# Performance work log

Hardware: AMD Instinct MI355X
Metric: run time of the kernel (lower is better)

## Reference

```python
import jax, jax.numpy as jnp
import numpy as np

# --- hash-grid / Field hyperparams (from init_kwargs defaults) ---
L = 16            # n_levels
F = 2             # n_features_per_level
LOG2_T = 19
T = 1 << LOG2_T   # hashmap size per level
NMIN = 16         # base_resolution
MAXRES = 512
SCALE = 1.0
HIDDEN = 32
OUT_DIM = 1
N = 2_000_000
B = float(np.exp(np.log(MAXRES * SCALE / NMIN) / (L - 1)))  # per_level_scale
PRIMES = jnp.array([1, 2654435761, 805459861], dtype=jnp.uint32)
# 8 corner offsets of the unit cube, (8,3)
CORNERS = jnp.array([[(c >> 0) & 1, (c >> 1) & 1, (c >> 2) & 1] for c in range(8)], dtype=jnp.uint32)


def hash_encode(xn, table):
    """xn: (N,3) in [0,1]; table: (L,T,F). Returns (N, L*F)."""
    feats = []
    for l in range(L):  # fixed small loop over levels
        s = NMIN * (B ** l) - 1.0          # tcnn-style grid scale
        pos = xn * s                        # (N,3)
        p0 = jnp.floor(pos)
        w = pos - p0                        # trilinear fracs, (N,3)
        p0i = p0.astype(jnp.uint32)
        corner = p0i[:, None, :] + CORNERS[None, :, :]          # (N,8,3)
        h = corner * PRIMES                                      # (N,8,3) uint32 wrap-mul
        idx = (h[..., 0] ^ h[..., 1] ^ h[..., 2]) & jnp.uint32(T - 1)  # (N,8)
        # trilinear weights per corner: prod over dims of w or (1-w)
        cw = jnp.where(CORNERS[None, :, :] == 1, w[:, None, :], 1.0 - w[:, None, :])
        cw = cw.prod(axis=-1)                                    # (N,8)
        g = table[l][idx.astype(jnp.int32)]                      # (N,8,F)
        feats.append(jnp.einsum('ncf,nc->nf', g, cw))            # (N,F)
    return jnp.concatenate(feats, axis=-1)                       # (N, L*F)


def setup_inputs() -> dict:
    key = jax.random.key(0)
    ks = jax.random.split(key, 8)
    x = jax.random.uniform(ks[0], (N, 3), jnp.float32)  # coords in [0,1) subset of [-scale,scale]
    table = jax.random.normal(ks[1], (L, T, F), jnp.float32) * 1e-2
    W0 = jax.random.normal(ks[2], (L * F + 3, HIDDEN), jnp.float32) * 0.1
    b0 = jnp.zeros((HIDDEN,), jnp.float32)
    W1 = jax.random.normal(ks[3], (HIDDEN, HIDDEN), jnp.float32) * 0.1
    b1 = jnp.zeros((HIDDEN,), jnp.float32)
    Wout = jax.random.normal(ks[4], (HIDDEN, OUT_DIM), jnp.float32) * 0.1
    bout = jnp.zeros((OUT_DIM,), jnp.float32)
    return {"x": x, "table": table, "W0": W0, "b0": b0, "W1": W1, "b1": b1, "Wout": Wout, "bout": bout}


def reference(x, table, W0, b0, W1, b1, Wout, bout):
    # density(): normalize coords to [0,1]
    xn = (x + SCALE) / (2.0 * SCALE)
    # back_prop=0: encoder sees detached coords
    h = hash_encode(jax.lax.stop_gradient(xn), table)   # (N, L*F)
    feat = jnp.concatenate([xn, h], axis=-1)            # (N, 35)  torch.cat([x, h], 1)
    h1 = jax.nn.elu(feat @ W0 + b0)
    h2 = jax.nn.elu(h1 @ W1 + b1)
    out = h2 @ Wout + bout                              # (N, 1)
    return out
```

## Files before the change

kernel.cpp:

```cpp
#include <hip/hip_runtime.h>
#include <hip/hip_fp16.h>
#include <cmath>

#define LVL   16
#define NDENSE 11
#define NHASH  (LVL - NDENSE)
#define TSIZE (1u << 19)
#define TMASK (TSIZE - 1u)
#define HID   32
#define PRIME1 2654435761u
#define PRIME2 805459861u
#define FSTRIDE 72

struct Scales { float s[LVL]; };
struct DenseInfo {
    int X0[NDENSE];
    int dim[NDENSE];
    int dimsq[NDENSE];
    int base[NDENSE];
    int eoff[NDENSE + 1];
};

typedef _Float16 f16x8 __attribute__((ext_vector_type(8)));
typedef float    f32x4 __attribute__((ext_vector_type(4)));
typedef float    f32x2 __attribute__((ext_vector_type(2)));
typedef unsigned u32x4 __attribute__((ext_vector_type(4)));

__device__ __forceinline__ float elu_f(float v) {
    return v > 0.0f ? v : expm1f(v);
}
__device__ __forceinline__ unsigned sel4(u32x4 v, unsigned s) {
    unsigned lo = (s & 1) ? v.y : v.x;
    unsigned hi = (s & 1) ? v.w : v.z;
    return (s & 2) ? hi : lo;
}
__device__ __forceinline__ unsigned hashed(unsigned cx, unsigned cy, unsigned cz) {
    return (cx ^ (cy * PRIME1) ^ (cz * PRIME2)) & TMASK;
}

__device__ __forceinline__ unsigned enc8(float v) {
    unsigned short t = __half_as_ushort(__float2half_rn(v * 0.0625f));
    unsigned m = (unsigned)(t & 0x7FFF) + 0x40u;
    return ((t >> 8) & 0x80u) | (m >> 7);
}
__device__ __forceinline__ float2 dec2(unsigned hw) {
    unsigned h2 = ((hw & 0x8000u) << 16) | ((hw & 0x7F00u) << 15)
                | ((hw & 0x80u)   << 8)  | ((hw & 0x7Fu)   << 7);
    __half2 hh; __builtin_memcpy(&hh, &h2, 4);
    return __half22float2(hh);
}

__global__ __launch_bounds__(256)
void convert_hash8(const f32x2* __restrict__ src, unsigned short* __restrict__ dst)
{
    int i = blockIdx.x * blockDim.x + threadIdx.x;
    if (i >= NHASH * (int)TSIZE) return;
    int l = NDENSE + i / (int)TSIZE;
    int s = i & (int)TMASK;
    f32x2 v = src[(size_t)l * TSIZE + s];
    dst[i] = (unsigned short)(enc8(v.x) | (enc8(v.y) << 8));
}

__global__ __launch_bounds__(256)
void dense_prep8(const float* __restrict__ table, u32x4* __restrict__ dtab,
                 DenseInfo di)
{
    int e = blockIdx.x * blockDim.x + threadIdx.x;
    if (e >= di.eoff[NDENSE]) return;
    int l = 0;
#pragma unroll
    for (int k = 1; k < NDENSE; ++k) if (e >= di.eoff[k]) l = k;
    int le = e - di.eoff[l];
    int D = di.dim[l];
    int ex = le % D; int r = le / D;
    int ey = r % D;  int ez = r / D;
    unsigned cx = (unsigned)(di.X0[l] + ex);
    unsigned cy = (unsigned)(di.X0[l] + ey);
    unsigned cz = (unsigned)(di.X0[l] + ez);
    const f32x2* __restrict__ tl = (const f32x2*)table + (size_t)l * TSIZE;
    f32x2 c0 = tl[hashed(cx,      cy,      cz)];
    f32x2 c1 = tl[hashed(cx + 1u, cy,      cz)];
    f32x2 c2 = tl[hashed(cx,      cy + 1u, cz)];
    f32x2 c3 = tl[hashed(cx + 1u, cy + 1u, cz)];
    f32x2 c4 = tl[hashed(cx,      cy,      cz + 1u)];
    f32x2 c5 = tl[hashed(cx + 1u, cy,      cz + 1u)];
    f32x2 c6 = tl[hashed(cx,      cy + 1u, cz + 1u)];
    f32x2 c7 = tl[hashed(cx + 1u, cy + 1u, cz + 1u)];
    u32x4 q;
    q.x = enc8(c0.x) | (enc8(c0.y) << 8) | (enc8(c1.x) << 16) | (enc8(c1.y) << 24);
    q.y = enc8(c2.x) | (enc8(c2.y) << 8) | (enc8(c3.x) << 16) | (enc8(c3.y) << 24);
    q.z = enc8(c4.x) | (enc8(c4.y) << 8) | (enc8(c5.x) << 16) | (enc8(c5.y) << 24);
    q.w = enc8(c6.x) | (enc8(c6.y) << 8) | (enc8(c7.x) << 16) | (enc8(c7.y) << 24);
    dtab[di.base[l] + le] = q;
}

__global__ void prep_frags(const float* __restrict__ W0, const float* __restrict__ W1,
                           const float* __restrict__ Wout, _Float16* __restrict__ frags)
{
    int idx = blockIdx.x * blockDim.x + threadIdx.x;
    if (idx >= 14*64*8) return;
    int f = idx >> 9;
    int rem = idx & 511;
    int lane = rem >> 3;
    int j = rem & 7;
    int q = lane >> 4;
    int nn = lane & 15;

    float w = 0.0f;
    bool lo;
    if (f < 8) {
        int part = f >> 2, kt = (f >> 1) & 1, nt = f & 1;
        int k = kt*32 + q*8 + j;
        int ncol = nt*16 + nn;
        float val = 0.0f;
        if (k < 32)      val = W0[(3 + k)  * HID + ncol];
        else if (k < 35) val = W0[(k - 32) * HID + ncol];
        else if (k < 38) val = W0[(k - 35) * HID + ncol];
        w = val; lo = (part == 1);
    } else if (f < 12) {
        int part = (f - 8) >> 1, nt = (f - 8) & 1;
        int k = q*8 + j;
        int ncol = nt*16 + nn;
        w = W1[k * HID + ncol]; lo = (part == 1);
    } else {
        int part = f - 12;
        int k = q*8 + j;
        w = (nn == 0) ? Wout[k] : 0.0f; lo = (part == 1);
    }
    _Float16 hi = (_Float16)w;
    frags[idx] = lo ? (_Float16)(w - (float)hi) : hi;
}

__global__ __launch_bounds__(256, 4)
void fused_mfma_kernel(const float* __restrict__ x, const u32x4* __restrict__ htab8,
                       const u32x4* __restrict__ dtab,
                       const float* __restrict__ b0, const float* __restrict__ b1,
                       const float* __restrict__ bout, const _Float16* __restrict__ fragbuf,
                       float* __restrict__ out, int n, Scales sc, DenseInfo di)
{
    __shared__ __attribute__((aligned(16))) _Float16 featL[256 * FSTRIDE];
    __shared__ __attribute__((aligned(16))) _Float16 h1h[4][16*32], h1l[4][16*32];
    __shared__ __attribute__((aligned(16))) _Float16 h2h[4][16*32], h2l[4][16*32];

    const int t = threadIdx.x;
    const int pbase = blockIdx.x * 256;
    const int p  = pbase + t;
    const int pc = p < n ? p : n - 1;

    const float xn0 = (x[3*pc+0] + 1.0f) * 0.5f;
    const float xn1 = (x[3*pc+1] + 1.0f) * 0.5f;
    const float xn2 = (x[3*pc+2] + 1.0f) * 0.5f;

    _Float16* row = &featL[t * FSTRIDE];
    {
        _Float16 h0 = (_Float16)xn0, h1_ = (_Float16)xn1, h2_ = (_Float16)xn2;
        row[32] = h0; row[33] = h1_; row[34] = h2_;
        row[35] = (_Float16)(xn0 - (float)h0);
        row[36] = (_Float16)(xn1 - (float)h1_);
        row[37] = (_Float16)(xn2 - (float)h2_);
#pragma unroll
        for (int k = 38; k < 64; ++k) row[k] = (_Float16)0.0f;
    }

#pragma unroll
    for (int l = 0; l < NDENSE; ++l) {
        const float s = sc.s[l];
        float px = xn0 * s, py = xn1 * s, pz = xn2 * s;
        float fx = floorf(px), fy = floorf(py), fz = floorf(pz);
        float wx = px - fx, wy = py - fy, wz = pz - fz;
        int D = di.dim[l], Dsq = di.dimsq[l], X0 = di.X0[l];
        int cx = (int)fx - X0, cy = (int)fy - X0, cz = (int)fz - X0;
        cx = min(max(cx, 0), D - 1);
        cy = min(max(cy, 0), D - 1);
        cz = min(max(cz, 0), D - 1);
        u32x4 Q = dtab[(size_t)(di.base[l] + cx + cy * D + cz * Dsq)];
        float2 a00 = dec2(Q.x & 0xFFFFu), a10 = dec2(Q.x >> 16);
        float2 a01 = dec2(Q.y & 0xFFFFu), a11 = dec2(Q.y >> 16);
        float2 c00 = dec2(Q.z & 0xFFFFu), c10 = dec2(Q.z >> 16);
        float2 c01 = dec2(Q.w & 0xFFFFu), c11 = dec2(Q.w >> 16);
        float ux = 1.0f - wx, uy = 1.0f - wy, uz = 1.0f - wz;
        float b0x = uy*(ux*a00.x + wx*a10.x) + wy*(ux*a01.x + wx*a11.x);
        float b0y = uy*(ux*a00.y + wx*a10.y) + wy*(ux*a01.y + wx*a11.y);
        float b1x = uy*(ux*c00.x + wx*c10.x) + wy*(ux*c01.x + wx*c11.x);
        float b1y = uy*(ux*c00.y + wx*c10.y) + wy*(ux*c01.y + wx*c11.y);
        row[2*l + 0] = (_Float16)(16.0f * (uz * b0x + wz * b1x));
        row[2*l + 1] = (_Float16)(16.0f * (uz * b0y + wz * b1y));
    }

#pragma unroll
    for (int l = NDENSE; l < LVL; ++l) {
        const u32x4* __restrict__ qt = htab8 + ((size_t)(l - NDENSE) * TSIZE >> 3);
        const float s = sc.s[l];
        float px = xn0 * s, py = xn1 * s, pz = xn2 * s;
        float fx = floorf(px), fy = floorf(py), fz = floorf(pz);
        float wx = px - fx, wy = py - fy, wz = pz - fz;
        unsigned x0 = (unsigned)fx, y0 = (unsigned)fy, z0 = (unsigned)fz;
        unsigned hy0 = y0 * PRIME1, hy1 = hy0 + PRIME1;
        unsigned hz0 = z0 * PRIME2, hz1 = hz0 + PRIME2;
        unsigned b00 = hy0 ^ hz0, b10 = hy1 ^ hz0, b01 = hy0 ^ hz1, b11 = hy1 ^ hz1;
        unsigned i0 = (x0 ^ b00) & TMASK;
        unsigned i1 = (x0 ^ b10) & TMASK;
        unsigned i2 = (x0 ^ b01) & TMASK;
        unsigned i3 = (x0 ^ b11) & TMASK;

        u32x4 Q0 = qt[i0 >> 3];
        u32x4 Q1 = qt[i1 >> 3];
        u32x4 Q2 = qt[i2 >> 3];
        u32x4 Q3 = qt[i3 >> 3];

        unsigned dm = (x0 ^ (x0 + 1u)) & TMASK;
        unsigned j0 = i0 ^ dm, j1 = i1 ^ dm, j2 = i2 ^ dm, j3 = i3 ^ dm;

        unsigned hc0, hc1, hc2, hc3;
        if ((x0 & 7u) == 7u) {
            u32x4 R0 = qt[j0 >> 3];
            u32x4 R1 = qt[j1 >> 3];
            u32x4 R2 = qt[j2 >> 3];
            u32x4 R3 = qt[j3 >> 3];
            unsigned d0 = sel4(R0, (j0 >> 1) & 3), d1 = sel4(R1, (j1 >> 1) & 3);
            unsigned d2 = sel4(R2, (j2 >> 1) & 3), d3 = sel4(R3, (j3 >> 1) & 3);
            hc0 = (j0 & 1) ? (d0 >> 16) : (d0 & 0xFFFFu);
            hc1 = (j1 & 1) ? (d1 >> 16) : (d1 & 0xFFFFu);
            hc2 = (j2 & 1) ? (d2 >> 16) : (d2 & 0xFFFFu);
            hc3 = (j3 & 1) ? (d3 >> 16) : (d3 & 0xFFFFu);
        } else {
            unsigned d0 = sel4(Q0, (j0 >> 1) & 3), d1 = sel4(Q1, (j1 >> 1) & 3);
            unsigned d2 = sel4(Q2, (j2 >> 1) & 3), d3 = sel4(Q3, (j3 >> 1) & 3);
            hc0 = (j0 & 1) ? (d0 >> 16) : (d0 & 0xFFFFu);
            hc1 = (j1 & 1) ? (d1 >> 16) : (d1 & 0xFFFFu);
            hc2 = (j2 & 1) ? (d2 >> 16) : (d2 & 0xFFFFu);
            hc3 = (j3 & 1) ? (d3 >> 16) : (d3 & 0xFFFFu);
        }
        unsigned e0 = sel4(Q0, (i0 >> 1) & 3), e1 = sel4(Q1, (i1 >> 1) & 3);
        unsigned e2 = sel4(Q2, (i2 >> 1) & 3), e3 = sel4(Q3, (i3 >> 1) & 3);
        unsigned ha0 = (i0 & 1) ? (e0 >> 16) : (e0 & 0xFFFFu);
        unsigned ha1 = (i1 & 1) ? (e1 >> 16) : (e1 & 0xFFFFu);
        unsigned ha2 = (i2 & 1) ? (e2 >> 16) : (e2 & 0xFFFFu);
        unsigned ha3 = (i3 & 1) ? (e3 >> 16) : (e3 & 0xFFFFu);

        float2 A0 = dec2(ha0), A1 = dec2(ha1), A2 = dec2(ha2), A3 = dec2(ha3);
        float2 C0 = dec2(hc0), C1 = dec2(hc1), C2 = dec2(hc2), C3 = dec2(hc3);
        float ux = 1.0f - wx, uy = 1.0f - wy, uz = 1.0f - wz;
        float w00 = uy*uz, w10 = wy*uz, w01 = uy*wz, w11 = wy*wz;
        float f0 = ux * (w00*A0.x + w10*A1.x + w01*A2.x + w11*A3.x)
                 + wx * (w00*C0.x + w10*C1.x + w01*C2.x + w11*C3.x);
        float f1 = ux * (w00*A0.y + w10*A1.y + w01*A2.y + w11*A3.y)
                 + wx * (w00*C0.y + w10*C1.y + w01*C2.y + w11*C3.y);

        row[2*l + 0] = (_Float16)(16.0f * f0);
        row[2*l + 1] = (_Float16)(16.0f * f1);
    }
    __syncthreads();

    const int l = t & 63, w = t >> 6;
    const int q = l >> 4, nn = l & 15;

    const f16x8* FB = (const f16x8*)fragbuf;
    f16x8 B0h00 = FB[0*64 + l], B0h01 = FB[1*64 + l];
    f16x8 B0h10 = FB[2*64 + l], B0h11 = FB[3*64 + l];
    f16x8 B0l00 = FB[4*64 + l], B0l01 = FB[5*64 + l];
    f16x8 B0l10 = FB[6*64 + l], B0l11 = FB[7*64 + l];
    f16x8 B1h0  = FB[8*64 + l], B1h1  = FB[9*64 + l];
    f16x8 B1l0  = FB[10*64 + l], B1l1 = FB[11*64 + l];
    f16x8 B2h   = FB[12*64 + l], B2l  = FB[13*64 + l];

    float bias00 = b0[nn], bias01 = b0[16 + nn];
    float bias10 = b1[nn], bias11 = b1[16 + nn];
    float biasO  = (nn == 0) ? bout[0] : 0.0f;

    _Float16* H1h = &h1h[w][0]; _Float16* H1l = &h1l[w][0];
    _Float16* H2h = &h2h[w][0]; _Float16* H2l = &h2l[w][0];

#pragma unroll
    for (int mt = 0; mt < 4; ++mt) {
        const int mrow = w*64 + mt*16 + nn;
        const _Float16* arow = &featL[mrow * FSTRIDE];

        f16x8 A0 = *(const f16x8*)(arow + q*8);
        f16x8 A1 = *(const f16x8*)(arow + 32 + q*8);
        f32x4 c0 = {bias00, bias00, bias00, bias00};
        f32x4 c1 = {bias01, bias01, bias01, bias01};
        c0 = __builtin_amdgcn_mfma_f32_16x16x32_f16(A0, B0h00, c0, 0, 0, 0);
        c0 = __builtin_amdgcn_mfma_f32_16x16x32_f16(A1, B0h10, c0, 0, 0, 0);
        c0 = __builtin_amdgcn_mfma_f32_16x16x32_f16(A0, B0l00, c0, 0, 0, 0);
        c0 = __builtin_amdgcn_mfma_f32_16x16x32_f16(A1, B0l10, c0, 0, 0, 0);
        c1 = __builtin_amdgcn_mfma_f32_16x16x32_f16(A0, B0h01, c1, 0, 0, 0);
        c1 = __builtin_amdgcn_mfma_f32_16x16x32_f16(A1, B0h11, c1, 0, 0, 0);
        c1 = __builtin_amdgcn_mfma_f32_16x16x32_f16(A0, B0l01, c1, 0, 0, 0);
        c1 = __builtin_amdgcn_mfma_f32_16x16x32_f16(A1, B0l11, c1, 0, 0, 0);

#pragma unroll
        for (int r = 0; r < 4; ++r) {
            int m = q*4 + r;
            float e0 = elu_f(c0[r]);
            _Float16 hh = (_Float16)e0;
            H1h[m*32 + nn]      = hh;
            H1l[m*32 + nn]      = (_Float16)(e0 - (float)hh);
            float e1 = elu_f(c1[r]);
            hh = (_Float16)e1;
            H1h[m*32 + 16 + nn] = hh;
            H1l[m*32 + 16 + nn] = (_Float16)(e1 - (float)hh);
        }

        f16x8 Ah = *(const f16x8*)(H1h + nn*32 + q*8);
        f16x8 Al = *(const f16x8*)(H1l + nn*32 + q*8);
        f32x4 d0 = {bias10, bias10, bias10, bias10};
        f32x4 d1 = {bias11, bias11, bias11, bias11};
        d0 = __builtin_amdgcn_mfma_f32_16x16x32_f16(Ah, B1h0, d0, 0, 0, 0);
        d0 = __builtin_amdgcn_mfma_f32_16x16x32_f16(Ah, B1l0, d0, 0, 0, 0);
        d0 = __builtin_amdgcn_mfma_f32_16x16x32_f16(Al, B1h0, d0, 0, 0, 0);
        d1 = __builtin_amdgcn_mfma_f32_16x16x32_f16(Ah, B1h1, d1, 0, 0, 0);
        d1 = __builtin_amdgcn_mfma_f32_16x16x32_f16(Ah, B1l1, d1, 0, 0, 0);
        d1 = __builtin_amdgcn_mfma_f32_16x16x32_f16(Al, B1h1, d1, 0, 0, 0);

#pragma unroll
        for (int r = 0; r < 4; ++r) {
            int m = q*4 + r;
            float e0 = elu_f(d0[r]);
            _Float16 hh = (_Float16)e0;
            H2h[m*32 + nn]      = hh;
            H2l[m*32 + nn]      = (_Float16)(e0 - (float)hh);
            float e1 = elu_f(d1[r]);
            hh = (_Float16)e1;
            H2h[m*32 + 16 + nn] = hh;
            H2l[m*32 + 16 + nn] = (_Float16)(e1 - (float)hh);
        }

        f16x8 A2h = *(const f16x8*)(H2h + nn*32 + q*8);
        f16x8 A2l = *(const f16x8*)(H2l + nn*32 + q*8);
        f32x4 c3 = {biasO, biasO, biasO, biasO};
        c3 = __builtin_amdgcn_mfma_f32_16x16x32_f16(A2h, B2h, c3, 0, 0, 0);
        c3 = __builtin_amdgcn_mfma_f32_16x16x32_f16(A2h, B2l, c3, 0, 0, 0);
        c3 = __builtin_amdgcn_mfma_f32_16x16x32_f16(A2l, B2h, c3, 0, 0, 0);

        if (nn == 0) {
            int pout = pbase + w*64 + mt*16 + q*4;
#pragma unroll
            for (int r = 0; r < 4; ++r)
                if (pout + r < n) out[pout + r] = c3[r];
        }
    }
}

__device__ __forceinline__ float2 enc_level_f32(float xn0, float xn1, float xn2, float s,
                                                const float2* __restrict__ tb)
{
    float px = xn0 * s, py = xn1 * s, pz = xn2 * s;
    float fx = floorf(px), fy = floorf(py), fz = floorf(pz);
    float wx = px - fx, wy = py - fy, wz = pz - fz;
    unsigned x0 = (unsigned)fx, y0 = (unsigned)fy, z0 = (unsigned)fz;
    unsigned hy0 = y0 * PRIME1, hy1 = hy0 + PRIME1;
    unsigned hz0 = z0 * PRIME2, hz1 = hz0 + PRIME2;
    unsigned b00 = hy0 ^ hz0, b10 = hy1 ^ hz0, b01 = hy0 ^ hz1, b11 = hy1 ^ hz1;
    float2 g000 = tb[( x0       ^ b00) & TMASK];
    float2 g100 = tb[((x0 + 1u) ^ b00) & TMASK];
    float2 g010 = tb[( x0       ^ b10) & TMASK];
    float2 g110 = tb[((x0 + 1u) ^ b10) & TMASK];
    float2 g001 = tb[( x0       ^ b01) & TMASK];
    float2 g101 = tb[((x0 + 1u) ^ b01) & TMASK];
    float2 g011 = tb[( x0       ^ b11) & TMASK];
    float2 g111 = tb[((x0 + 1u) ^ b11) & TMASK];
    float ux = 1.0f - wx, uy = 1.0f - wy, uz = 1.0f - wz;
    float c00 = uy*uz, c10 = wy*uz, c01 = uy*wz, c11 = wy*wz;
    float f0 = ux * (c00*g000.x + c10*g010.x + c01*g001.x + c11*g011.x)
             + wx * (c00*g100.x + c10*g110.x + c01*g101.x + c11*g111.x);
    float f1 = ux * (c00*g000.y + c10*g010.y + c01*g001.y + c11*g011.y)
             + wx * (c00*g100.y + c10*g110.y + c01*g101.y + c11*g111.y);
    return make_float2(f0, f1);
}

__global__ __launch_bounds__(256, 4)
void fused_fp32_kernel(const float* __restrict__ x, const float* __restrict__ table,
                       const float* __restrict__ W0, const float* __restrict__ b0,
                       const float* __restrict__ W1, const float* __restrict__ b1,
                       const float* __restrict__ Wout, const float* __restrict__ bout,
                       float* __restrict__ out, int n, Scales sc)
{
    int tid = blockIdx.x * blockDim.x + threadIdx.x;
    if (tid >= n) return;
    float xn0 = (x[3*tid+0] + 1.0f) * 0.5f;
    float xn1 = (x[3*tid+1] + 1.0f) * 0.5f;
    float xn2 = (x[3*tid+2] + 1.0f) * 0.5f;
    float acc[HID];
#pragma unroll
    for (int j = 0; j < HID; ++j)
        acc[j] = b0[j] + xn0 * W0[0*HID + j] + xn1 * W0[1*HID + j] + xn2 * W0[2*HID + j];
#pragma unroll
    for (int lv = 0; lv < LVL; ++lv) {
        const float2* tb = (const float2*)table + (size_t)lv * TSIZE;
        float2 f = enc_level_f32(xn0, xn1, xn2, sc.s[lv], tb);
        const float* w0r0 = W0 + (3 + 2*lv) * HID;
        const float* w0r1 = W0 + (4 + 2*lv) * HID;
#pragma unroll
        for (int j = 0; j < HID; ++j)
            acc[j] += f.x * w0r0[j] + f.y * w0r1[j];
    }
#pragma unroll
    for (int j = 0; j < HID; ++j) acc[j] = elu_f(acc[j]);
    float acc2[HID];
#pragma unroll
    for (int j = 0; j < HID; ++j) acc2[j] = b1[j];
#pragma unroll
    for (int k = 0; k < HID; ++k) {
        float hk = acc[k];
        const float* w1r = W1 + k * HID;
#pragma unroll
        for (int j = 0; j < HID; ++j) acc2[j] += hk * w1r[j];
    }
    float o = bout[0];
#pragma unroll
    for (int k = 0; k < HID; ++k) o += elu_f(acc2[k]) * Wout[k];
    out[tid] = o;
}

extern "C" void kernel_launch(void* const* d_in, const int* in_sizes, int n_in,
                              void* d_out, int out_size, void* d_ws, size_t ws_size,
                              hipStream_t stream)
{
    const float* x    = (const float*)d_in[0];
    const float* tb   = (const float*)d_in[1];
    const float* W0   = (const float*)d_in[2];
    const float* b0   = (const float*)d_in[3];
    const float* W1   = (const float*)d_in[4];
    const float* b1   = (const float*)d_in[5];
    const float* Wout = (const float*)d_in[6];
    const float* bo   = (const float*)d_in[7];
    float* out = (float*)d_out;

    int n = in_sizes[0] / 3;

    Scales sc;
    DenseInfo di;
    double B = exp(log(32.0) / 15.0);
    {
        int base = 0, ecum = 0;
        for (int l = 0; l < LVL; ++l) {
            double sd = 16.0 * pow(B, (double)l) - 1.0;
            sc.s[l] = (float)sd;
            if (l < NDENSE) {
                int X0   = (int)floor(0.5 * sd) - 2; if (X0 < 0) X0 = 0;
                int Xmax = (int)ceil(sd) + 2;
                int dim  = Xmax - X0 + 1;
                di.X0[l] = X0; di.dim[l] = dim; di.dimsq[l] = dim * dim;
                di.base[l] = base; di.eoff[l] = ecum;
                base += dim * dim * dim;
                ecum += dim * dim * dim;
            }
        }
        di.eoff[NDENSE] = ecum;
    }

    const size_t dense_bytes = (size_t)di.eoff[NDENSE] * 16;
    const size_t hash8_bytes = (size_t)NHASH * TSIZE * 2;
    const size_t frag_bytes  = 14 * 64 * 8 * sizeof(_Float16);
    int block = 256;
    int pgrid = (n + block - 1) / block;

    if (ws_size >= dense_bytes + hash8_bytes + frag_bytes) {
        u32x4*          dtab  = (u32x4*)d_ws;
        unsigned short* htab8 = (unsigned short*)((char*)d_ws + dense_bytes);
        _Float16*       frags = (_Float16*)((char*)d_ws + dense_bytes + hash8_bytes);
        int hgrid = (NHASH * (int)TSIZE + block - 1) / block;
        convert_hash8<<<hgrid, block, 0, stream>>>((const f32x2*)tb, htab8);
        int dgrid = (di.eoff[NDENSE] + block - 1) / block;
        dense_prep8<<<dgrid, block, 0, stream>>>(tb, dtab, di);
        prep_frags<<<28, 256, 0, stream>>>(W0, W1, Wout, frags);
        fused_mfma_kernel<<<pgrid, block, 0, stream>>>(x, (const u32x4*)htab8, dtab,
                                                       b0, b1, bo, frags, out, n, sc, di);
    } else {
        fused_fp32_kernel<<<pgrid, block, 0, stream>>>(x, tb, W0, b0, W1, b1, Wout, bo, out, n, sc);
    }
}
```

Baseline: 523.0 us.

## Merge table-prep kernels into one launch and extend dense levels to 13

Combines the hash-table 8-bit conversion, the dense corner-packed table build and the MLP fragment prep into a single kernel, which saves two launches and lets the independent prep work overlap. It also raises the number of levels served from a precomputed dense corner table from 11 to 13, so only 3 levels still need random hashed gathers in the main kernel. The trade-off is a larger dense table to build and read each call, since levels 11-12 have many more cells. The workspace must also be big enough for the bigger table, otherwise the code falls back to the fp32 kernel.

After: 527.7 us. No clear change (+0.9%).

```diff
diff --git a/kernel.cpp b/kernel.cpp
--- a/kernel.cpp
+++ b/kernel.cpp
@@ -3,7 +3,7 @@
 #include <cmath>
 
 #define LVL   16
-#define NDENSE 11
+#define NDENSE 13
 #define NHASH  (LVL - NDENSE)
 #define TSIZE (1u << 19)
 #define TMASK (TSIZE - 1u)
@@ -51,53 +51,53 @@
 }
 
 __global__ __launch_bounds__(256)
-void convert_hash8(const f32x2* __restrict__ src, unsigned short* __restrict__ dst)
+void prep_all(const float* __restrict__ table,
+              const float* __restrict__ W0, const float* __restrict__ W1,
+              const float* __restrict__ Wout,
+              unsigned short* __restrict__ htab8, u32x4* __restrict__ dtab,
+              _Float16* __restrict__ frags, DenseInfo di)
 {
-    int i = blockIdx.x * blockDim.x + threadIdx.x;
-    if (i >= NHASH * (int)TSIZE) return;
-    int l = NDENSE + i / (int)TSIZE;
-    int s = i & (int)TMASK;
-    f32x2 v = src[(size_t)l * TSIZE + s];
-    dst[i] = (unsigned short)(enc8(v.x) | (enc8(v.y) << 8));
-}
-
-__global__ __launch_bounds__(256)
-void dense_prep8(const float* __restrict__ table, u32x4* __restrict__ dtab,
-                 DenseInfo di)
-{
-    int e = blockIdx.x * blockDim.x + threadIdx.x;
-    if (e >= di.eoff[NDENSE]) return;
-    int l = 0;
-#pragma unroll
-    for (int k = 1; k < NDENSE; ++k) if (e >= di.eoff[k]) l = k;
-    int le = e - di.eoff[l];
-    int D = di.dim[l];
-    int ex = le % D; int r = le / D;
-    int ey = r % D;  int ez = r / D;
-    unsigned cx = (unsigned)(di.X0[l] + ex);
-    unsigned cy = (unsigned)(di.X0[l] + ey);
-    unsigned cz = (unsigned)(di.X0[l] + ez);
-    const f32x2* __restrict__ tl = (const f32x2*)table + (size_t)l * TSIZE;
-    f32x2 c0 = tl[hashed(cx,      cy,      cz)];
-    f32x2 c1 = tl[hashed(cx + 1u, cy,      cz)];
-    f32x2 c2 = tl[hashed(cx,      cy + 1u, cz)];
-    f32x2 c3 = tl[hashed(cx + 1u, cy + 1u, cz)];
-    f32x2 c4 = tl[hashed(cx,      cy,      cz + 1u)];
-    f32x2 c5 = tl[hashed(cx + 1u, cy,      cz + 1u)];
-    f32x2 c6 = tl[hashed(cx,      cy + 1u, cz + 1u)];
-    f32x2 c7 = tl[hashed(cx + 1u, cy + 1u, cz + 1u)];
-    u32x4 q;
-    q.x = enc8(c0.x) | (enc8(c0.y) << 8) | (enc8(c1.x) << 16) | (enc8(c1.y) << 24);
-    q.y = enc8(c2.x) | (enc8(c2.y) << 8) | (enc8(c3.x) << 16) | (enc8(c3.y) << 24);
-    q.z = enc8(c4.x) | (enc8(c4.y) << 8) | (enc8(c5.x) << 16) | (enc8(c5.y) << 24);
-    q.w = enc8(c6.x) | (enc8(c6.y) << 8) | (enc8(c7.x) << 16) | (enc8(c7.y) << 24);
-    dtab[di.base[l] + le] = q;
-}
-
-__global__ void prep_frags(const float* __restrict__ W0, const float* __restrict__ W1,
-                           const float* __restrict__ Wout, _Float16* __restrict__ frags)
-{
-    int idx = blockIdx.x * blockDim.x + threadIdx.x;
+    const int NH = NHASH * (int)TSIZE;
+    const int NC = di.eoff[NDENSE];
+    int tid = blockIdx.x * blockDim.x + threadIdx.x;
+
+    if (tid < NH) {
+        int l = NDENSE + tid / (int)TSIZE;
+        int s = tid & (int)TMASK;
+        f32x2 v = ((const f32x2*)table)[(size_t)l * TSIZE + s];
+        htab8[tid] = (unsigned short)(enc8(v.x) | (enc8(v.y) << 8));
+        return;
+    }
+    int e = tid - NH;
+    if (e < NC) {
+        int l = 0;
+#pragma unroll
+        for (int k = 1; k < NDENSE; ++k) if (e >= di.eoff[k]) l = k;
+        int le = e - di.eoff[l];
+        int D = di.dim[l];
+        int ex = le % D; int r = le / D;
+        int ey = r % D;  int ez = r / D;
+        unsigned cx = (unsigned)(di.X0[l] + ex);
+        unsigned cy = (unsigned)(di.X0[l] + ey);
+        unsigned cz = (unsigned)(di.X0[l] + ez);
+        const f32x2* __restrict__ tl = (const f32x2*)table + (size_t)l * TSIZE;
+        f32x2 c0 = tl[hashed(cx,      cy,      cz)];
+        f32x2 c1 = tl[hashed(cx + 1u, cy,      cz)];
+        f32x2 c2 = tl[hashed(cx,      cy + 1u, cz)];
+        f32x2 c3 = tl[hashed(cx + 1u, cy + 1u, cz)];
+        f32x2 c4 = tl[hashed(cx,      cy,      cz + 1u)];
+        f32x2 c5 = tl[hashed(cx + 1u, cy,      cz + 1u)];
+        f32x2 c6 = tl[hashed(cx,      cy + 1u, cz + 1u)];
+        f32x2 c7 = tl[hashed(cx + 1u, cy + 1u, cz + 1u)];
+        u32x4 q;
+        q.x = enc8(c0.x) | (enc8(c0.y) << 8) | (enc8(c1.x) << 16) | (enc8(c1.y) << 24);
+        q.y = enc8(c2.x) | (enc8(c2.y) << 8) | (enc8(c3.x) << 16) | (enc8(c3.y) << 24);
+        q.z = enc8(c4.x) | (enc8(c4.y) << 8) | (enc8(c5.x) << 16) | (enc8(c5.y) << 24);
+        q.w = enc8(c6.x) | (enc8(c6.y) << 8) | (enc8(c7.x) << 16) | (enc8(c7.y) << 24);
+        dtab[di.base[l] + le] = q;
+        return;
+    }
+    int idx = e - NC;
     if (idx >= 14*64*8) return;
     int f = idx >> 9;
     int rem = idx & 511;
@@ -105,7 +105,6 @@
     int j = rem & 7;
     int q = lane >> 4;
     int nn = lane & 15;
-
     float w = 0.0f;
     bool lo;
     if (f < 8) {
@@ -460,12 +459,10 @@
         u32x4*          dtab  = (u32x4*)d_ws;
         unsigned short* htab8 = (unsigned short*)((char*)d_ws + dense_bytes);
         _Float16*       frags = (_Float16*)((char*)d_ws + dense_bytes + hash8_bytes);
-        int hgrid = (NHASH * (int)TSIZE + block - 1) / block;
-        convert_hash8<<<hgrid, block, 0, stream>>>((const f32x2*)tb, htab8);
-        int dgrid = (di.eoff[NDENSE] + block - 1) / block;
-        dense_prep8<<<dgrid, block, 0, stream>>>(tb, dtab, di);
-        prep_frags<<<28, 256, 0, stream>>>(W0, W1, Wout, frags);
-        fused_mfma_kernel<<<pgrid, block, 0, stream>>>(x, (const u32x4*)htab8, dtab,
+        long long total = (long long)NHASH * TSIZE + di.eoff[NDENSE] + 14*64*8;
+        int pg = (int)((total + block - 1) / block);
+        prep_all<<<pg, block, 0, stream>>>(tb, W0, W1, Wout, htab8, (u32x4*)dtab, frags, di);
+        fused_mfma_kernel<<<pgrid, block, 0, stream>>>(x, (const u32x4*)htab8, (const u32x4*)dtab,
                                                        b0, b1, bo, frags, out, n, sc, di);
     } else {
         fused_fp32_kernel<<<pgrid, block, 0, stream>>>(x, tb, W0, b0, W1, b1, Wout, bo, out, n, sc);
```
